# Kernel tuning notes

Hardware: AMD Instinct MI355X
Metric: run time of the kernel (lower is better)

## Reference

```python
import jax, jax.numpy as jnp
import numpy as np

B, T, E = 4, 2048, 1024
H, D = 8, 128  # num_query_heads, head_dimension (single shared KV head -> MQA)


def sinusoidal_pe(length, dim, dtype=jnp.float32):
    """Standard additive sinusoidal PE table of shape (length, dim)."""
    pos = jnp.arange(length, dtype=jnp.float32)[:, None]            # (L, 1)
    inv_freq = jnp.exp(-jnp.log(jnp.float32(10000.0)) * (jnp.arange(0, dim, 2, dtype=jnp.float32) / dim))
    ang = pos * inv_freq[None, :]                                    # (L, dim//2)
    pe = jnp.zeros((length, dim), dtype=jnp.float32)
    pe = pe.at[:, 0::2].set(jnp.sin(ang)).at[:, 1::2].set(jnp.cos(ang))
    return pe.astype(dtype)


def setup_inputs() -> dict:
    key = jax.random.key(0)
    kx, kq, kk, kv, ko = jax.random.split(key, 5)
    s = 0.02  # weight init scale
    return {
        "x": jax.random.normal(kx, (B, T, E), dtype=jnp.float32),
        "Wq": jax.random.normal(kq, (H * D, E), dtype=jnp.float32) * s,
        "Wk": jax.random.normal(kk, (D, E), dtype=jnp.float32) * s,
        "Wv": jax.random.normal(kv, (D, E), dtype=jnp.float32) * s,
        "Wo": jax.random.normal(ko, (E, H * D), dtype=jnp.float32) * s,
    }


def reference(x, Wq, Wk, Wv, Wo):
    Bv, Tv, Ev = x.shape
    scale = 1.0 / jnp.sqrt(jnp.float32(D)).astype(x.dtype)

    q = (x @ Wq.T).reshape(Bv, Tv, H, D)        # (B, T, H, D)
    k = (x @ Wk.T).reshape(Bv, Tv, 1, D)        # (B, T, 1, D) single KV head
    v = (x @ Wv.T).reshape(Bv, Tv, 1, D)

    # positional_embedding applied along axis -2 (as in (.., seq, dim) layout):
    # for k (B,T,1,D) the -2 axis has length 1 -> adds pe[0];
    # for q after permute (B,H,T,D) the -2 axis is T -> full table.
    k = k + sinusoidal_pe(1, D, k.dtype)        # broadcast over (B, T)

    q = jnp.transpose(q, (0, 2, 1, 3))          # (B, H, T, D)
    k1 = k[:, :, 0, :]                          # (B, T, D) shared KV head
    v1 = v[:, :, 0, :]                          # (B, T, D)

    q = q + sinusoidal_pe(Tv, D, q.dtype)[None, None]

    # MQA SDPA: broadcast single K/V head across H query heads
    scores = jnp.einsum("bhtd,bsd->bhts", q, k1) * scale   # (B, H, T, T)
    causal = jnp.tril(jnp.ones((Tv, Tv), dtype=bool))
    scores = jnp.where(causal[None, None], scores, jnp.finfo(scores.dtype).min)
    probs = jax.nn.softmax(scores, axis=-1)
    attn = jnp.einsum("bhts,bsd->bhtd", probs, v1)          # (B, H, T, D)

    out = jnp.transpose(attn, (0, 2, 1, 3)).reshape(Bv, Tv, H * D)
    return out @ Wo.T                                        # (B, T, E)
```

## Files before the change

kernel.cpp:

```cpp
#include <hip/hip_runtime.h>
#include <hip/hip_bf16.h>
#include <cstdint>
#include <cstddef>

#define B_ 4
#define T_ 2048
#define E_ 1024
#define H_ 8
#define D_ 128

typedef unsigned short u16;
typedef __bf16 bf16x8 __attribute__((ext_vector_type(8)));
typedef float f32x4 __attribute__((ext_vector_type(4)));

#define MFMA16(a, b, c) __builtin_amdgcn_mfma_f32_16x16x32_bf16((a), (b), (c), 0, 0, 0)

#if defined(__has_builtin)
#if __has_builtin(__builtin_amdgcn_global_load_lds)
#define HAVE_GLL 1
#endif
#if __has_builtin(__builtin_amdgcn_exp2f)
#define HAVE_EXP2 1
#endif
#endif

__device__ __forceinline__ void gload_lds16(const u16* g, u16* l) {
#ifdef HAVE_GLL
  __builtin_amdgcn_global_load_lds(
      (const __attribute__((address_space(1))) void*)g,
      (__attribute__((address_space(3))) void*)l, 16, 0, 0);
#else
  int lane = threadIdx.x & 63;
  *(uint4*)(l + lane * 8) = *(const uint4*)(g);
#endif
}

__device__ __forceinline__ float fexp2(float x) {
#ifdef HAVE_EXP2
  return __builtin_amdgcn_exp2f(x);
#else
  return __expf(x * 0.69314718056f);
#endif
}

__device__ __forceinline__ u16 f2bf(float f) {
  union { float f; uint32_t u; } a; a.f = f;
  uint32_t u = a.u;
  uint32_t r = (u + 0x7fffu + ((u >> 16) & 1u)) >> 16;
  return (u16)r;
}

__device__ __forceinline__ uint32_t pkbf(float lo, float hi) {
  uint32_t r;
  asm volatile("v_cvt_pk_bf16_f32 %0, %1, %2" : "=v"(r) : "v"(lo), "v"(hi));
  return r;
}

__device__ __forceinline__ void cvt4(const float* __restrict__ s, u16* __restrict__ d, int i4) {
  float4 v = *(const float4*)(s + (size_t)i4 * 4);
  uint2 o;
  o.x = (uint32_t)f2bf(v.x) | ((uint32_t)f2bf(v.y) << 16);
  o.y = (uint32_t)f2bf(v.z) | ((uint32_t)f2bf(v.w) << 16);
  *(uint2*)(d + (size_t)i4 * 4) = o;
}

__global__ __launch_bounds__(256) void prep_kernel(
    const float* __restrict__ x,  const float* __restrict__ Wq,
    const float* __restrict__ Wk, const float* __restrict__ Wv,
    const float* __restrict__ Wo,
    u16* __restrict__ xbf, u16* __restrict__ Wcat, u16* __restrict__ Wobf,
    float* __restrict__ pe)
{
  int id = blockIdx.x * 256 + threadIdx.x;
  if (id < 2097152) { cvt4(x, xbf, id); return; }
  id -= 2097152;
  if (id < 262144) { cvt4(Wq, Wcat, id); return; }
  id -= 262144;
  if (id < 32768) { cvt4(Wk, Wcat + 1048576, id); return; }
  id -= 32768;
  if (id < 32768) { cvt4(Wv, Wcat + 1179648, id); return; }
  id -= 32768;
  if (id < 262144) { cvt4(Wo, Wobf, id); return; }
  id -= 262144;
  int t = id >> 6, i = id & 63;
  float f = expf(-logf(10000.0f) * (float)i / 64.0f);
  float ang = (float)t * f;
  pe[t * 128 + 2 * i]     = sinf(ang);
  pe[t * 128 + 2 * i + 1] = cosf(ang);
}

template<int MODE>
__global__ __launch_bounds__(256) void gemm_nt(
    const u16* __restrict__ A, const u16* __restrict__ Bm,
    u16* __restrict__ Qb, u16* __restrict__ Kb, u16* __restrict__ VTb,
    const float* __restrict__ pe, float* __restrict__ Cout, int K)
{
  __shared__ u16 Al[128 * 32];
  __shared__ u16 Bl[128 * 32];
  const int t = threadIdx.x;
  const int l = t & 63, w = t >> 6;
  const int wr = w >> 1, wc = w & 1;
  const int bm = blockIdx.x * 128, bn = blockIdx.y * 128;
  const int lr = l & 15, lg = l >> 4;

  const int srow = w * 32 + (l >> 2);
  const int scol = (l & 3) * 8;
  const u16* gA0 = A + (size_t)(bm + srow) * K + scol;
  const u16* gB0 = Bm + (size_t)(bn + srow) * K + scol;
  u16* lA0 = &Al[(w * 32) * 32];
  u16* lA1 = &Al[(w * 32 + 16) * 32];
  u16* lB0 = &Bl[(w * 32) * 32];
  u16* lB1 = &Bl[(w * 32 + 16) * 32];
  const size_t r16 = (size_t)16 * K;

  f32x4 acc[4][4] = {};

  for (int k0 = 0; k0 < K; k0 += 32) {
    gload_lds16(gA0 + k0, lA0);
    gload_lds16(gA0 + r16 + k0, lA1);
    gload_lds16(gB0 + k0, lB0);
    gload_lds16(gB0 + r16 + k0, lB1);
    __syncthreads();
    bf16x8 af[4], bfr[4];
    #pragma unroll
    for (int m = 0; m < 4; ++m)
      af[m] = *(const bf16x8*)(&Al[(wr * 64 + m * 16 + lr) * 32 + lg * 8]);
    #pragma unroll
    for (int n = 0; n < 4; ++n)
      bfr[n] = *(const bf16x8*)(&Bl[(wc * 64 + n * 16 + lr) * 32 + lg * 8]);
    __builtin_amdgcn_s_setprio(1);
    #pragma unroll
    for (int m = 0; m < 4; ++m) {
      #pragma unroll
      for (int n = 0; n < 4; ++n)
        acc[m][n] = MFMA16(af[m], bfr[n], acc[m][n]);
    }
    __builtin_amdgcn_s_setprio(0);
    __syncthreads();
  }

  const float qscale = 0.12752869468f;
  #pragma unroll
  for (int m = 0; m < 4; ++m) {
    #pragma unroll
    for (int n = 0; n < 4; ++n) {
      const int gm0 = bm + wr * 64 + m * 16 + lg * 4;
      const int gn = bn + wc * 64 + n * 16 + lr;
      if constexpr (MODE == 0) {
        const int b = gm0 >> 11, tq0 = gm0 & (T_ - 1);
        if (gn < 1024) {
          int hh = gn >> 7, d = gn & 127;
          #pragma unroll
          for (int r = 0; r < 4; ++r)
            Qb[(((size_t)(b * H_ + hh) * T_ + tq0 + r) << 7) + d] =
                f2bf((acc[m][n][r] + pe[((tq0 + r) << 7) + d]) * qscale);
        } else if (gn < 1152) {
          int d = gn - 1024;
          #pragma unroll
          for (int r = 0; r < 4; ++r)
            Kb[((size_t)(gm0 + r) << 7) + d] = f2bf(acc[m][n][r] + (float)(d & 1));
        } else {
          int d = gn - 1152;
          uint2 pk;
          pk.x = pkbf(acc[m][n][0], acc[m][n][1]);
          pk.y = pkbf(acc[m][n][2], acc[m][n][3]);
          *(uint2*)(VTb + ((size_t)(b * 128 + d) << 11) + tq0) = pk;
        }
      } else {
        #pragma unroll
        for (int r = 0; r < 4; ++r)
          Cout[(size_t)(gm0 + r) * 1024 + gn] = acc[m][n][r];
      }
    }
  }
}

__global__ __launch_bounds__(512) void attn_kernel(
    const u16* __restrict__ Qb, const u16* __restrict__ Kb,
    const u16* __restrict__ VTg, u16* __restrict__ Ob)
{
  __shared__ u16 Kl[128 * 128];
  __shared__ u16 VTl[128 * 128];
  __shared__ u16 Pl[8 * 16 * 128];
  const int t = threadIdx.x;
  const int l = t & 63, w = t >> 6;
  const int lr = l & 15, lg = l >> 4;
  const int sw = lr & 7;
  const int p = blockIdx.x, b = blockIdx.y;
  const int h = w;
  const int q0A = p * 16, q0B = (127 - p) * 16;
  const int ntA = (q0A + 16 + 127) >> 7, ntB = (q0B + 16 + 127) >> 7;

  const u16* qbA = Qb + (((size_t)(b * H_ + h) * T_ + q0A + lr) << 7);
  const u16* qbB = Qb + (((size_t)(b * H_ + h) * T_ + q0B + lr) << 7);
  bf16x8 qfA[4], qfB[4];
  #pragma unroll
  for (int kc = 0; kc < 4; ++kc) {
    qfA[kc] = *(const bf16x8*)(qbA + kc * 32 + lg * 8);
    qfB[kc] = *(const bf16x8*)(qbB + kc * 32 + lg * 8);
  }

  float mA = -3e38f, mB = -3e38f, lA = 0.f, lB = 0.f;
  f32x4 oA[8] = {}, oB[8] = {};
  u16* pw = &Pl[w * 16 * 128];

  auto process = [&](f32x4 (&s)[8], float& m, float& lsum, f32x4 (&o)[8],
                     int q0F, int kt, bool masked) {
    float pv[32];
    float pm = -3e38f;
    if (masked) {
      const int qv = q0F + lr;
      #pragma unroll
      for (int kvf = 0; kvf < 8; ++kvf) {
        #pragma unroll
        for (int r = 0; r < 4; ++r) {
          int kv = kt * 128 + kvf * 16 + lg * 4 + r;
          float sv = (kv <= qv) ? s[kvf][r] : -3e38f;
          pv[kvf * 4 + r] = sv;
          pm = fmaxf(pm, sv);
        }
      }
    } else {
      #pragma unroll
      for (int kvf = 0; kvf < 8; ++kvf) {
        #pragma unroll
        for (int r = 0; r < 4; ++r) {
          float sv = s[kvf][r];
          pv[kvf * 4 + r] = sv;
          pm = fmaxf(pm, sv);
        }
      }
    }
    pm = fmaxf(pm, __shfl_xor(pm, 16));
    pm = fmaxf(pm, __shfl_xor(pm, 32));
    float mn;
    if (__all(pm <= m + 11.5f)) {
      mn = m;
    } else {
      mn = fmaxf(m, pm);
      float corr = fexp2(m - mn);
      lsum *= corr;
      #pragma unroll
      for (int df = 0; df < 8; ++df) {
        #pragma unroll
        for (int r = 0; r < 4; ++r) o[df][r] *= corr;
      }
      m = mn;
    }
    float ps = 0.f;
    #pragma unroll
    for (int i = 0; i < 32; ++i) {
      pv[i] = fexp2(pv[i] - mn);
      ps += pv[i];
    }
    ps += __shfl_xor(ps, 16);
    ps += __shfl_xor(ps, 32);
    lsum += ps;
    #pragma unroll
    for (int kvf = 0; kvf < 8; ++kvf) {
      uint2 pk;
      pk.x = pkbf(pv[kvf * 4 + 0], pv[kvf * 4 + 1]);
      pk.y = pkbf(pv[kvf * 4 + 2], pv[kvf * 4 + 3]);
      int un = ((2 * kvf + (lg >> 1)) ^ sw) * 8 + (lg & 1) * 4;
      *(uint2*)(&pw[lr * 128 + un]) = pk;
    }
    __builtin_amdgcn_s_setprio(1);
    #pragma unroll
    for (int kc = 0; kc < 4; ++kc) {
      bf16x8 pf = *(const bf16x8*)(&pw[lr * 128 + ((4 * kc + lg) ^ sw) * 8]);
      #pragma unroll
      for (int df = 0; df < 8; ++df) {
        bf16x8 vf = *(const bf16x8*)(&VTl[((df * 16 + lr) << 7) + ((4 * kc + lg) ^ sw) * 8]);
        o[df] = MFMA16(vf, pf, o[df]);
      }
    }
    __builtin_amdgcn_s_setprio(0);
  };

  for (int kt = 0; kt < ntB; ++kt) {
    #pragma unroll
    for (int it = 0; it < 4; ++it) {
      int cc = it * 512 + t;
      int row = cc >> 4, u = cc & 15;
      int off = (row << 7) + ((u ^ (row & 7)) << 3);
      *(uint4*)(&Kl[off]) =
          *(const uint4*)(Kb + ((size_t)(b * T_ + kt * 128 + row) << 7) + u * 8);
      *(uint4*)(&VTl[off]) =
          *(const uint4*)(VTg + ((size_t)(b * 128 + row) << 11) + kt * 128 + u * 8);
    }
    __syncthreads();

    const bool actA = kt < ntA;
    f32x4 sA[8] = {}, sB[8] = {};
    __builtin_amdgcn_s_setprio(1);
    #pragma unroll
    for (int kvf = 0; kvf < 8; ++kvf) {
      bf16x8 kf[4];
      #pragma unroll
      for (int kc = 0; kc < 4; ++kc)
        kf[kc] = *(const bf16x8*)(&Kl[((kvf * 16 + lr) << 7) + ((4 * kc + lg) ^ sw) * 8]);
      #pragma unroll
      for (int kc = 0; kc < 4; ++kc)
        sB[kvf] = MFMA16(kf[kc], qfB[kc], sB[kvf]);
      if (actA) {
        #pragma unroll
        for (int kc = 0; kc < 4; ++kc)
          sA[kvf] = MFMA16(kf[kc], qfA[kc], sA[kvf]);
      }
    }
    __builtin_amdgcn_s_setprio(0);
    process(sB, mB, lB, oB, q0B, kt, kt * 128 + 127 > q0B);
    if (actA) process(sA, mA, lA, oA, q0A, kt, kt * 128 + 127 > q0A);
    __syncthreads();
  }

  float rA = 1.0f / lA, rB = 1.0f / lB;
  #pragma unroll
  for (int df = 0; df < 8; ++df) {
    uint2 pk;
    pk.x = pkbf(oB[df][0] * rB, oB[df][1] * rB);
    pk.y = pkbf(oB[df][2] * rB, oB[df][3] * rB);
    *(uint2*)(Ob + ((size_t)(b * T_ + q0B + lr) << 10) + h * 128 + df * 16 + lg * 4) = pk;
    pk.x = pkbf(oA[df][0] * rA, oA[df][1] * rA);
    pk.y = pkbf(oA[df][2] * rA, oA[df][3] * rA);
    *(uint2*)(Ob + ((size_t)(b * T_ + q0A + lr) << 10) + h * 128 + df * 16 + lg * 4) = pk;
  }
}

extern "C" void kernel_launch(void* const* d_in, const int* in_sizes, int n_in,
                              void* d_out, int out_size, void* d_ws, size_t ws_size,
                              hipStream_t stream) {
  const float* x  = (const float*)d_in[0];
  const float* Wq = (const float*)d_in[1];
  const float* Wk = (const float*)d_in[2];
  const float* Wv = (const float*)d_in[3];
  const float* Wo = (const float*)d_in[4];

  char* ws = (char*)d_ws;
  size_t off = 0;
  auto alloc = [&](size_t bytes) {
    char* p = ws + off;
    off += (bytes + 255) & ~(size_t)255;
    return p;
  };
  u16*   xbf  = (u16*)  alloc(8388608ull * 2);
  u16*   Wcat = (u16*)  alloc(1310720ull * 2);
  u16*   Wobf = (u16*)  alloc(1048576ull * 2);
  float* pe   = (float*)alloc(262144ull * 4);
  u16*   Qbuf = (u16*)  alloc(8388608ull * 2);
  u16*   Kbuf = (u16*)  alloc(1048576ull * 2);
  u16*   VTbuf= (u16*)  alloc(1048576ull * 2);
  u16*   Abuf = (u16*)  alloc(8388608ull * 2);

  prep_kernel<<<11008, 256, 0, stream>>>(x, Wq, Wk, Wv, Wo, xbf, Wcat, Wobf, pe);

  gemm_nt<0><<<dim3(64, 10), 256, 0, stream>>>(xbf, Wcat, Qbuf, Kbuf, VTbuf, pe, nullptr, 1024);
  attn_kernel<<<dim3(64, 4), 512, 0, stream>>>(Qbuf, Kbuf, VTbuf, Abuf);
  gemm_nt<1><<<dim3(64, 8), 256, 0, stream>>>(Abuf, Wobf, nullptr, nullptr, nullptr, nullptr,
                                              (float*)d_out, 1024);
}
```

Before: 149.9 us.

## Double-buffer K/V tiles in attention with async global-to-LDS loads and 64-wide tiles

The attention kernel now processes the key/value sequence in tiles of 64 instead of 128 and keeps two LDS buffers for K and V^T. The next tile is prefetched with direct global-to-LDS loads while the current one is being computed, with the XOR swizzle moved onto the global source address. This is meant to hide global load latency behind the MFMA and softmax work, and to cut wasted work on the causal diagonal through the finer tile size. In exchange there are more loop iterations and more softmax rescale and reduction steps per query. Correctness depends on the barrier waiting for the async LDS writes to finish.

```diff
diff --git a/kernel.cpp b/kernel.cpp
--- a/kernel.cpp
+++ b/kernel.cpp
@@ -179,9 +179,9 @@
     const u16* __restrict__ Qb, const u16* __restrict__ Kb,
     const u16* __restrict__ VTg, u16* __restrict__ Ob)
 {
-  __shared__ u16 Kl[128 * 128];
-  __shared__ u16 VTl[128 * 128];
-  __shared__ u16 Pl[8 * 16 * 128];
+  __shared__ u16 Kl[2][64 * 128];
+  __shared__ u16 VTl[2][128 * 64];
+  __shared__ u16 Pl[8 * 16 * 64];
   const int t = threadIdx.x;
   const int l = t & 63, w = t >> 6;
   const int lr = l & 15, lg = l >> 4;
@@ -189,7 +189,26 @@
   const int p = blockIdx.x, b = blockIdx.y;
   const int h = w;
   const int q0A = p * 16, q0B = (127 - p) * 16;
-  const int ntA = (q0A + 16 + 127) >> 7, ntB = (q0B + 16 + 127) >> 7;
+  const int ntA = (q0A + 16 + 63) >> 6, ntB = (q0B + 16 + 63) >> 6;
+
+  auto stage = [&](int kt, int s) {
+    #pragma unroll
+    for (int c = 0; c < 2; ++c) {
+      int n = c * 512 + t;
+      {
+        int row = n >> 4, ul = n & 15;
+        int ug = ul ^ (row & 7);
+        gload_lds16(Kb + ((size_t)(b * T_ + kt * 64 + row) << 7) + ug * 8,
+                    &Kl[s][(size_t)(c * 512 + w * 64) * 8]);
+      }
+      {
+        int row = n >> 3, ul = n & 7;
+        int ug = ul ^ (row & 7);
+        gload_lds16(VTg + ((size_t)(b * 128 + row) << 11) + kt * 64 + ug * 8,
+                    &VTl[s][(size_t)(c * 512 + w * 64) * 8]);
+      }
+    }
+  };
 
   const u16* qbA = Qb + (((size_t)(b * H_ + h) * T_ + q0A + lr) << 7);
   const u16* qbB = Qb + (((size_t)(b * H_ + h) * T_ + q0B + lr) << 7);
@@ -202,19 +221,19 @@
 
   float mA = -3e38f, mB = -3e38f, lA = 0.f, lB = 0.f;
   f32x4 oA[8] = {}, oB[8] = {};
-  u16* pw = &Pl[w * 16 * 128];
-
-  auto process = [&](f32x4 (&s)[8], float& m, float& lsum, f32x4 (&o)[8],
-                     int q0F, int kt, bool masked) {
-    float pv[32];
+  u16* pw = &Pl[w * 16 * 64];
+
+  auto process = [&](f32x4 (&s)[4], float& m, float& lsum, f32x4 (&o)[8],
+                     int q0F, int kt, bool masked, const u16* vtl) {
+    float pv[16];
     float pm = -3e38f;
     if (masked) {
       const int qv = q0F + lr;
       #pragma unroll
-      for (int kvf = 0; kvf < 8; ++kvf) {
+      for (int kvf = 0; kvf < 4; ++kvf) {
         #pragma unroll
         for (int r = 0; r < 4; ++r) {
-          int kv = kt * 128 + kvf * 16 + lg * 4 + r;
+          int kv = kt * 64 + kvf * 16 + lg * 4 + r;
           float sv = (kv <= qv) ? s[kvf][r] : -3e38f;
           pv[kvf * 4 + r] = sv;
           pm = fmaxf(pm, sv);
@@ -222,7 +241,7 @@
       }
     } else {
       #pragma unroll
-      for (int kvf = 0; kvf < 8; ++kvf) {
+      for (int kvf = 0; kvf < 4; ++kvf) {
         #pragma unroll
         for (int r = 0; r < 4; ++r) {
           float sv = s[kvf][r];
@@ -249,7 +268,7 @@
     }
     float ps = 0.f;
     #pragma unroll
-    for (int i = 0; i < 32; ++i) {
+    for (int i = 0; i < 16; ++i) {
       pv[i] = fexp2(pv[i] - mn);
       ps += pv[i];
     }
@@ -257,48 +276,42 @@
     ps += __shfl_xor(ps, 32);
     lsum += ps;
     #pragma unroll
-    for (int kvf = 0; kvf < 8; ++kvf) {
+    for (int kvf = 0; kvf < 4; ++kvf) {
       uint2 pk;
       pk.x = pkbf(pv[kvf * 4 + 0], pv[kvf * 4 + 1]);
       pk.y = pkbf(pv[kvf * 4 + 2], pv[kvf * 4 + 3]);
       int un = ((2 * kvf + (lg >> 1)) ^ sw) * 8 + (lg & 1) * 4;
-      *(uint2*)(&pw[lr * 128 + un]) = pk;
+      *(uint2*)(&pw[lr * 64 + un]) = pk;
     }
     __builtin_amdgcn_s_setprio(1);
     #pragma unroll
-    for (int kc = 0; kc < 4; ++kc) {
-      bf16x8 pf = *(const bf16x8*)(&pw[lr * 128 + ((4 * kc + lg) ^ sw) * 8]);
+    for (int kc = 0; kc < 2; ++kc) {
+      bf16x8 pf = *(const bf16x8*)(&pw[lr * 64 + ((4 * kc + lg) ^ sw) * 8]);
       #pragma unroll
       for (int df = 0; df < 8; ++df) {
-        bf16x8 vf = *(const bf16x8*)(&VTl[((df * 16 + lr) << 7) + ((4 * kc + lg) ^ sw) * 8]);
+        bf16x8 vf = *(const bf16x8*)(&vtl[(df * 16 + lr) * 64 + ((4 * kc + lg) ^ sw) * 8]);
         o[df] = MFMA16(vf, pf, o[df]);
       }
     }
     __builtin_amdgcn_s_setprio(0);
   };
 
+  stage(0, 0);
+  __syncthreads();
+
   for (int kt = 0; kt < ntB; ++kt) {
-    #pragma unroll
-    for (int it = 0; it < 4; ++it) {
-      int cc = it * 512 + t;
-      int row = cc >> 4, u = cc & 15;
-      int off = (row << 7) + ((u ^ (row & 7)) << 3);
-      *(uint4*)(&Kl[off]) =
-          *(const uint4*)(Kb + ((size_t)(b * T_ + kt * 128 + row) << 7) + u * 8);
-      *(uint4*)(&VTl[off]) =
-          *(const uint4*)(VTg + ((size_t)(b * 128 + row) << 11) + kt * 128 + u * 8);
-    }
-    __syncthreads();
+    const int cur = kt & 1;
+    if (kt + 1 < ntB) stage(kt + 1, cur ^ 1);
 
     const bool actA = kt < ntA;
-    f32x4 sA[8] = {}, sB[8] = {};
+    f32x4 sA[4] = {}, sB[4] = {};
     __builtin_amdgcn_s_setprio(1);
     #pragma unroll
-    for (int kvf = 0; kvf < 8; ++kvf) {
+    for (int kvf = 0; kvf < 4; ++kvf) {
       bf16x8 kf[4];
       #pragma unroll
       for (int kc = 0; kc < 4; ++kc)
-        kf[kc] = *(const bf16x8*)(&Kl[((kvf * 16 + lr) << 7) + ((4 * kc + lg) ^ sw) * 8]);
+        kf[kc] = *(const bf16x8*)(&Kl[cur][((kvf * 16 + lr) << 7) + ((4 * kc + lg) ^ sw) * 8]);
       #pragma unroll
       for (int kc = 0; kc < 4; ++kc)
         sB[kvf] = MFMA16(kf[kc], qfB[kc], sB[kvf]);
@@ -309,8 +322,8 @@
       }
     }
     __builtin_amdgcn_s_setprio(0);
-    process(sB, mB, lB, oB, q0B, kt, kt * 128 + 127 > q0B);
-    if (actA) process(sA, mA, lA, oA, q0A, kt, kt * 128 + 127 > q0A);
+    process(sB, mB, lB, oB, q0B, kt, kt * 64 + 63 > q0B, &VTl[cur][0]);
+    if (actA) process(sA, mA, lA, oA, q0A, kt, kt * 64 + 63 > q0A, &VTl[cur][0]);
     __syncthreads();
   }
 
```

Result: faster. 145.6 us (-2.9%).
